# Optimization experiments

Hardware: AMD Instinct MI355X
Metric: run time of the kernel (lower is better)

The kernel has to match this reference:

```python
import jax, jax.numpy as jnp
import numpy as np

N, E, F, CUTOFF = 50000, 500000, 64, 5.0
EPS_CN, EPS_LN = 1e-8, 1e-5


def _xavier(k, shape):
    lim = float(np.sqrt(6.0 / (shape[0] + shape[1])))
    return jax.random.uniform(k, shape, jnp.float32, -lim, lim)


def setup_inputs() -> dict:
    key = jax.random.key(0)
    ks = jax.random.split(key, 20)
    vn = jax.random.normal(ks[5], (E, 3), jnp.float32)
    vn = vn / jnp.linalg.norm(vn, axis=-1, keepdims=True)  # unit direction vectors
    return {
        "node_s": jax.random.normal(ks[0], (N, 1, F), jnp.float32),
        "node_v": jax.random.normal(ks[1], (N, 3, F), jnp.float32),
        "edge_s": jax.random.normal(ks[2], (E, 1, F), jnp.float32),
        "edge_v": jax.random.normal(ks[3], (E, 3, F), jnp.float32),
        "dist": jax.random.uniform(ks[4], (E, 1), jnp.float32) * CUTOFF,
        "vctr_norm": vn,
        "src": jax.random.randint(ks[6], (E,), 0, N),
        "dst": jax.random.randint(ks[7], (E,), 0, N),
        "W_nn": _xavier(ks[8], (2 * F, F)), "b_nn": jnp.zeros((F,), jnp.float32),
        "W_ep": _xavier(ks[9], (F, F)), "b_ep": jnp.zeros((F,), jnp.float32),
        "W_g1": _xavier(ks[10], (F, F)), "b_g1": jnp.zeros((F,), jnp.float32),
        "W_g2": _xavier(ks[11], (F, F)), "b_g2": jnp.zeros((F,), jnp.float32),
        "W_ev": _xavier(ks[12], (F, 3 * F)), "b_ev": jnp.zeros((3 * F,), jnp.float32),
        "W_nvout": _xavier(ks[13], (F, 3 * F)),
        "W_nvc": _xavier(ks[14], (2 * F, F)), "b_nvc": jnp.zeros((F,), jnp.float32),
        "W_nvp": _xavier(ks[15], (F, 2 * F)),
        "W_nsp": _xavier(ks[16], (F, 2 * F)), "b_nsp": jnp.zeros((2 * F,), jnp.float32),
        "ln_gamma": jnp.ones((F,), jnp.float32), "ln_beta": jnp.zeros((F,), jnp.float32),
        "cn_scale": jnp.ones((F,), jnp.float32),
    }


def reference(node_s, node_v, edge_s, edge_v, dist, vctr_norm, src, dst,
              W_nn, b_nn, W_ep, b_ep, W_g1, b_g1, W_g2, b_g2, W_ev, b_ev,
              W_nvout, W_nvc, b_nvc, W_nvp, W_nsp, b_nsp, ln_gamma, ln_beta, cn_scale):
    n_nodes = node_s.shape[0]
    # cosine cutoff [E,1]
    c = 0.5 * (jnp.cos(jnp.pi * dist / CUTOFF) + 1.0) * (dist < CUTOFF).astype(dist.dtype)
    # ---- edge scalar update (gather src/dst, small MLPs) ----
    nn_in = jnp.concatenate([node_s[src], node_s[dst]], axis=-1)        # [E,1,2F]
    node_neighbors = nn_in @ W_nn + b_nn                                # [E,1,F]
    edge_message = node_neighbors * (edge_s @ W_ep + b_ep)              # [E,1,F]
    h = jax.nn.silu(edge_message @ W_g1 + b_g1)                         # GateMLP hidden
    es_upd = (h @ W_g2 + b_g2) * c[..., None]                           # [E,1,F]
    # ---- edge vector update ----
    vch = es_upd @ W_ev + b_ev                                          # [E,1,3F]
    nch, ech, rch = jnp.split(vch, 3, axis=-1)
    ev_upd = node_v[src] * nch + edge_v * ech + vctr_norm[..., None] * rch  # [E,3,F]
    ev_upd = ev_upd * c[..., None]
    # ---- scatter-mean to destination nodes ----
    deg = jax.ops.segment_sum(jnp.ones((src.shape[0],), node_s.dtype), dst, num_segments=n_nodes)
    denom = jnp.maximum(deg, 1.0)[:, None, None]
    n_ev = jax.ops.segment_sum(ev_upd, dst, num_segments=n_nodes) / denom  # [N,3,F]
    n_es = jax.ops.segment_sum(es_upd, dst, num_segments=n_nodes) / denom  # [N,1,F]
    # ---- node vector update ----
    nv_o1, nv_o2, nv_o3 = jnp.split(n_ev @ W_nvout, 3, axis=-1)          # each [N,3,F]
    v_in = jnp.concatenate([n_es, jnp.linalg.norm(nv_o3, axis=1, keepdims=True)], axis=-1)  # [N,1,2F]
    v_channel = v_in @ W_nvc + b_nvc                                     # [N,1,F]
    nv_upd = nv_o1 * v_channel + nv_o2                                   # [N,3,F]
    # ---- node scalar update ----
    nvp1, nvp2 = jnp.split(nv_upd @ W_nvp, 2, axis=-1)                   # [N,3,F] each
    ns1, ns2 = jnp.split(jax.nn.silu(n_es @ W_nsp + b_nsp), 2, axis=-1)  # [N,1,F] each
    nv_dot = jnp.sum(nvp1 * nvp2, axis=1, keepdims=True)                 # [N,1,F]
    ns_upd = nv_dot * ns1 + ns2                                          # [N,1,F]
    # ---- residuals + norms ----
    node_s_out = ns_upd + node_s
    node_v_out = nv_upd + node_v
    edge_s_out = es_upd + edge_s
    edge_v_out = ev_upd + edge_v
    # CoorsNorm: normalize over the 3D axis, learnable per-channel scale
    vnorm = jnp.linalg.norm(node_v_out, axis=1, keepdims=True)
    node_v_out = node_v_out / jnp.maximum(vnorm, EPS_CN) * cn_scale
    # LayerNorm over feature dim
    mu = jnp.mean(node_s_out, axis=-1, keepdims=True)
    var = jnp.var(node_s_out, axis=-1, keepdims=True)
    node_s_out = (node_s_out - mu) / jnp.sqrt(var + EPS_LN) * ln_gamma + ln_beta
    return node_s_out, node_v_out, edge_s_out, edge_v_out
```

## Files before the change

### kernel.cpp

```cpp
#include <hip/hip_runtime.h>
#include <hip/hip_bf16.h>
#include <math.h>

typedef __attribute__((ext_vector_type(8))) short bf16x8;
typedef __attribute__((ext_vector_type(4))) float f32x4;

#define MFMA16(a, b, c) __builtin_amdgcn_mfma_f32_16x16x32_bf16((a), (b), (c), 0, 0, 0)

__device__ __forceinline__ float silu_f(float x) { return x / (1.0f + expf(-x)); }

__device__ __forceinline__ unsigned short f2bf(float f) {
  union { __hip_bfloat16 h; unsigned short u; } c;
  c.h = __float2bfloat16(f);
  return c.u;
}
__device__ __forceinline__ unsigned pk2(float a, float b) {
  return (unsigned)f2bf(a) | ((unsigned)f2bf(b) << 16);
}
__device__ __forceinline__ float bfu(unsigned short u) {
  union { unsigned u32; float f; } c;
  c.u32 = (unsigned)u << 16;
  return c.f;
}

__device__ __forceinline__ bf16x8 ld_act(const unsigned short* buf, int strideB, int ks, int lane) {
  int row = lane & 15;
  int off = row * strideB + ks * 64 + ((lane >> 4) << 4);
  off ^= (row & 7) << 4;
  return *(const bf16x8*)((const char*)buf + off);
}

__device__ __forceinline__ bf16x8 ld_w(const unsigned short* Wt, int rowbase, int strideB, int ks, int lane) {
  return *(const bf16x8*)((const char*)Wt + (size_t)(rowbase + (lane & 15)) * strideB + ks * 64 + ((lane >> 4) << 4));
}

__global__ void wprep_all(const float* __restrict__ W_nn, const float* __restrict__ W_ep,
                          const float* __restrict__ W_g1, const float* __restrict__ W_g2,
                          const float* __restrict__ W_ev,
                          unsigned short* __restrict__ wnn_t, unsigned short* __restrict__ wep_t,
                          unsigned short* __restrict__ wg1_t, unsigned short* __restrict__ wg2_t,
                          unsigned short* __restrict__ wev_t) {
  int idx = blockIdx.x * 256 + threadIdx.x;
  if (idx < 8192) {
    int n = idx >> 7, k = idx & 127;
    wnn_t[idx] = f2bf(W_nn[k * 64 + n]);
  } else if (idx < 12288) {
    int t = idx - 8192; int n = t >> 6, k = t & 63;
    wep_t[t] = f2bf(W_ep[k * 64 + n]);
  } else if (idx < 16384) {
    int t = idx - 12288; int n = t >> 6, k = t & 63;
    wg1_t[t] = f2bf(W_g1[k * 64 + n]);
  } else if (idx < 20480) {
    int t = idx - 16384; int n = t >> 6, k = t & 63;
    wg2_t[t] = f2bf(W_g2[k * 64 + n]);
  } else if (idx < 32768) {
    int t = idx - 20480; int n = t >> 6, k = t & 63;
    wev_t[t] = f2bf(W_ev[k * 192 + n]);
  }
}

__global__ void hist_kernel(const int* __restrict__ dst, int* __restrict__ cnt, int E) {
  int i = blockIdx.x * blockDim.x + threadIdx.x;
  if (i < E) atomicAdd(&cnt[dst[i]], 1);
}

__global__ __launch_bounds__(1024) void scan_kernel(int* __restrict__ cnt,
                                                    int* __restrict__ rowstart, int N) {
  __shared__ int wsum[16];
  const int tid = threadIdx.x;
  const int wv = tid >> 6;
  int carry = 0;
  for (int base = 0; base < N; base += 1024) {
    int i = base + tid;
    int v = (i < N) ? cnt[i] : 0;
    int x = v;
    #pragma unroll
    for (int o = 1; o < 64; o <<= 1) {
      int y = __shfl_up(x, o);
      if ((tid & 63) >= o) x += y;
    }
    if ((tid & 63) == 63) wsum[wv] = x;
    __syncthreads();
    if (tid < 16) {
      int s = wsum[tid];
      #pragma unroll
      for (int o = 1; o < 16; o <<= 1) {
        int y = __shfl_up(s, o);
        if (tid >= o) s += y;
      }
      wsum[tid] = s;
    }
    __syncthreads();
    int woff = (wv > 0) ? wsum[wv - 1] : 0;
    if (i < N) {
      int excl = carry + woff + x - v;
      rowstart[i] = excl;
      cnt[i] = excl;
    }
    carry += wsum[15];
    __syncthreads();
  }
  if (tid == 0) rowstart[N] = carry;
}

__global__ void scatter_kernel(const int* __restrict__ dst, int* __restrict__ cursor,
                               int* __restrict__ elist, int E) {
  int i = blockIdx.x * blockDim.x + threadIdx.x;
  if (i < E) {
    int pos = atomicAdd(&cursor[dst[i]], 1);
    elist[pos] = i;
  }
}

__global__ __launch_bounds__(256, 8) void edge_kernel(
    const float* __restrict__ node_s, const float* __restrict__ node_v,
    const float* __restrict__ edge_s, const float* __restrict__ edge_v,
    const float* __restrict__ dist,   const float* __restrict__ vctr,
    const int* __restrict__ src,      const int* __restrict__ dst,
    const unsigned short* __restrict__ wnn_t, const float* __restrict__ b_nn,
    const unsigned short* __restrict__ wep_t, const float* __restrict__ b_ep,
    const unsigned short* __restrict__ wg1_t, const float* __restrict__ b_g1,
    const unsigned short* __restrict__ wg2_t, const float* __restrict__ b_g2,
    const unsigned short* __restrict__ wev_t, const float* __restrict__ b_ev,
    float* __restrict__ es_out, float* __restrict__ ev_out,
    unsigned short* __restrict__ raw_es, unsigned short* __restrict__ raw_ev,
    int use_raw, int E, int n_tiles)
{
  __shared__ __align__(16) unsigned short lds[4 * 2048];
  const int wid  = threadIdx.x >> 6;
  const int lane = threadIdx.x & 63;
  const int tile = blockIdx.x * 4 + wid;
  if (tile >= n_tiles) return;
  const int ebase = tile * 16;
  unsigned short* bufA = lds + wid * 2048;

  const int m  = lane & 15;
  const int nb = lane >> 4;

  {
    const int sm = lane >> 5;
    const int kk = lane & 31;
    #pragma unroll
    for (int p = 0; p < 8; ++p) {
      int le = p * 2 + sm;
      int e = ebase + le; if (e >= E) e = E - 1;
      int s = src[e], d = dst[e];
      float2 vs = *(const float2*)(node_s + (size_t)s * 64 + 2 * kk);
      float2 vd = *(const float2*)(node_s + (size_t)d * 64 + 2 * kk);
      unsigned swz = (le & 7) << 4;
      *(unsigned*)((char*)bufA + ((le * 256 + kk * 4) ^ swz))       = pk2(vs.x, vs.y);
      *(unsigned*)((char*)bufA + ((le * 256 + 128 + kk * 4) ^ swz)) = pk2(vd.x, vd.y);
    }
  }
  __builtin_amdgcn_wave_barrier();

  const int e = (ebase + m < E) ? ebase + m : E - 1;
  const float dd_ = dist[e];
  const float cc = (dd_ < 5.0f) ? 0.5f * (cosf(3.14159265358979f * dd_ * 0.2f) + 1.0f) : 0.0f;
  const int s_nd = src[e];

  const f32x4 z4 = {0.0f, 0.0f, 0.0f, 0.0f};
  const unsigned swzm = (m & 7) << 4;

  bf16x8 a0 = ld_act(bufA, 256, 0, lane), a1 = ld_act(bufA, 256, 1, lane);
  bf16x8 a2 = ld_act(bufA, 256, 2, lane), a3 = ld_act(bufA, 256, 3, lane);

  const float* esrow = edge_s + (size_t)e * 64;
  bf16x8 b0, b1;
  {
    const int k8 = (lane >> 4) << 3;
    f32x4 p0 = *(const f32x4*)(esrow + k8);
    f32x4 p1 = *(const f32x4*)(esrow + k8 + 4);
    f32x4 q0 = *(const f32x4*)(esrow + 32 + k8);
    f32x4 q1 = *(const f32x4*)(esrow + 32 + k8 + 4);
    union { bf16x8 v; uint4 u; } cb;
    cb.u.x = pk2(p0.x, p0.y); cb.u.y = pk2(p0.z, p0.w);
    cb.u.z = pk2(p1.x, p1.y); cb.u.w = pk2(p1.z, p1.w);
    b0 = cb.v;
    cb.u.x = pk2(q0.x, q0.y); cb.u.y = pk2(q0.z, q0.w);
    cb.u.z = pk2(q1.x, q1.y); cb.u.w = pk2(q1.z, q1.w);
    b1 = cb.v;
  }
  __builtin_amdgcn_wave_barrier();

  #pragma unroll
  for (int nt = 0; nt < 4; ++nt) {
    f32x4 aN = z4, aP = z4;
    aN = MFMA16(ld_w(wnn_t, nt * 16, 256, 0, lane), a0, aN);
    aN = MFMA16(ld_w(wnn_t, nt * 16, 256, 1, lane), a1, aN);
    aN = MFMA16(ld_w(wnn_t, nt * 16, 256, 2, lane), a2, aN);
    aN = MFMA16(ld_w(wnn_t, nt * 16, 256, 3, lane), a3, aN);
    aP = MFMA16(ld_w(wep_t, nt * 16, 128, 0, lane), b0, aP);
    aP = MFMA16(ld_w(wep_t, nt * 16, 128, 1, lane), b1, aP);
    f32x4 bn = *(const f32x4*)(b_nn + nt * 16 + nb * 4);
    f32x4 bp = *(const f32x4*)(b_ep + nt * 16 + nb * 4);
    float e0 = (aN.x + bn.x) * (aP.x + bp.x);
    float e1 = (aN.y + bn.y) * (aP.y + bp.y);
    float e2 = (aN.z + bn.z) * (aP.z + bp.z);
    float e3 = (aN.w + bn.w) * (aP.w + bp.w);
    uint2 w2; w2.x = pk2(e0, e1); w2.y = pk2(e2, e3);
    *(uint2*)((char*)bufA + ((m * 128 + nt * 32 + nb * 8) ^ swzm)) = w2;
  }
  __builtin_amdgcn_wave_barrier();

  bf16x8 c0 = ld_act(bufA, 128, 0, lane), c1 = ld_act(bufA, 128, 1, lane);
  __builtin_amdgcn_wave_barrier();
  #pragma unroll
  for (int nt = 0; nt < 4; ++nt) {
    f32x4 aH = z4;
    aH = MFMA16(ld_w(wg1_t, nt * 16, 128, 0, lane), c0, aH);
    aH = MFMA16(ld_w(wg1_t, nt * 16, 128, 1, lane), c1, aH);
    f32x4 bg = *(const f32x4*)(b_g1 + nt * 16 + nb * 4);
    uint2 w2;
    w2.x = pk2(silu_f(aH.x + bg.x), silu_f(aH.y + bg.y));
    w2.y = pk2(silu_f(aH.z + bg.z), silu_f(aH.w + bg.w));
    *(uint2*)((char*)bufA + ((m * 128 + nt * 32 + nb * 8) ^ swzm)) = w2;
  }
  __builtin_amdgcn_wave_barrier();

  bf16x8 d0 = ld_act(bufA, 128, 0, lane), d1 = ld_act(bufA, 128, 1, lane);
  __builtin_amdgcn_wave_barrier();
  float* eorow = es_out + (size_t)e * 64;
  #pragma unroll
  for (int nt = 0; nt < 4; ++nt) {
    f32x4 aS = z4;
    aS = MFMA16(ld_w(wg2_t, nt * 16, 128, 0, lane), d0, aS);
    aS = MFMA16(ld_w(wg2_t, nt * 16, 128, 1, lane), d1, aS);
    f32x4 bg = *(const f32x4*)(b_g2 + nt * 16 + nb * 4);
    float u0 = (aS.x + bg.x) * cc, u1 = (aS.y + bg.y) * cc;
    float u2 = (aS.z + bg.z) * cc, u3 = (aS.w + bg.w) * cc;
    const int n0 = nt * 16 + nb * 4;
    uint2 w2; w2.x = pk2(u0, u1); w2.y = pk2(u2, u3);
    *(uint2*)((char*)bufA + ((m * 128 + nt * 32 + nb * 8) ^ swzm)) = w2;
    if (use_raw) *(uint2*)(raw_es + (size_t)e * 64 + n0) = w2;
    if (ebase + m < E) {
      f32x4 r = *(const f32x4*)(esrow + n0);
      f32x4 o; o.x = u0 + r.x; o.y = u1 + r.y; o.z = u2 + r.z; o.w = u3 + r.w;
      __builtin_nontemporal_store(o, (f32x4*)(eorow + n0));
    }
  }
  __builtin_amdgcn_wave_barrier();

  bf16x8 g0 = ld_act(bufA, 128, 0, lane), g1f = ld_act(bufA, 128, 1, lane);
  const float* nvb = node_v + (size_t)s_nd * 192;
  const float* evb = edge_v + (size_t)e * 192;
  float* eob = ev_out + (size_t)e * 192;
  float vnn0 = vctr[e * 3], vnn1 = vctr[e * 3 + 1], vnn2 = vctr[e * 3 + 2];
  const bool live = (ebase + m < E);
  #pragma unroll
  for (int nt = 0; nt < 4; ++nt) {
    f32x4 aN = z4, aE = z4, aR = z4;
    aN = MFMA16(ld_w(wev_t,        nt * 16, 128, 0, lane), g0,  aN);
    aN = MFMA16(ld_w(wev_t,        nt * 16, 128, 1, lane), g1f, aN);
    aE = MFMA16(ld_w(wev_t,  64 + nt * 16, 128, 0, lane), g0,  aE);
    aE = MFMA16(ld_w(wev_t,  64 + nt * 16, 128, 1, lane), g1f, aE);
    aR = MFMA16(ld_w(wev_t, 128 + nt * 16, 128, 0, lane), g0,  aR);
    aR = MFMA16(ld_w(wev_t, 128 + nt * 16, 128, 1, lane), g1f, aR);
    const int n0 = nt * 16 + nb * 4;
    f32x4 bv0 = *(const f32x4*)(b_ev + n0);
    f32x4 bv1 = *(const f32x4*)(b_ev + 64 + n0);
    f32x4 bv2 = *(const f32x4*)(b_ev + 128 + n0);
    aN.x += bv0.x; aN.y += bv0.y; aN.z += bv0.z; aN.w += bv0.w;
    aE.x += bv1.x; aE.y += bv1.y; aE.z += bv1.z; aE.w += bv1.w;
    aR.x += bv2.x; aR.y += bv2.y; aR.z += bv2.z; aR.w += bv2.w;
    #pragma unroll
    for (int dd = 0; dd < 3; ++dd) {
      const float vn = (dd == 0) ? vnn0 : (dd == 1) ? vnn1 : vnn2;
      f32x4 nv = *(const f32x4*)(nvb + dd * 64 + n0);
      f32x4 ev = __builtin_nontemporal_load((const f32x4*)(evb + dd * 64 + n0));
      float eu0 = (nv.x * aN.x + ev.x * aE.x + vn * aR.x) * cc;
      float eu1 = (nv.y * aN.y + ev.y * aE.y + vn * aR.y) * cc;
      float eu2 = (nv.z * aN.z + ev.z * aE.z + vn * aR.z) * cc;
      float eu3 = (nv.w * aN.w + ev.w * aE.w + vn * aR.w) * cc;
      if (use_raw) {
        uint2 r; r.x = pk2(eu0, eu1); r.y = pk2(eu2, eu3);
        *(uint2*)(raw_ev + (size_t)e * 192 + dd * 64 + n0) = r;
      }
      if (live) {
        f32x4 o; o.x = eu0 + ev.x; o.y = eu1 + ev.y; o.z = eu2 + ev.z; o.w = eu3 + ev.w;
        __builtin_nontemporal_store(o, (f32x4*)(eob + dd * 64 + n0));
      }
    }
  }
}

__device__ __forceinline__ void ld4(const float* p, float o[4]) {
  f32x4 v = *(const f32x4*)p;
  o[0] = v.x; o[1] = v.y; o[2] = v.z; o[3] = v.w;
}

__global__ __launch_bounds__(256) void node_kernel(
    const float* __restrict__ node_s, const float* __restrict__ node_v,
    const float* __restrict__ edge_s, const float* __restrict__ edge_v,
    const float* __restrict__ es_r,   const float* __restrict__ ev_r,
    const unsigned short* __restrict__ raw_es, const unsigned short* __restrict__ raw_ev,
    const int* __restrict__ rowstart, const int* __restrict__ elist, int use_raw,
    const float* __restrict__ W_nvout,
    const float* __restrict__ W_nvc, const float* __restrict__ b_nvc,
    const float* __restrict__ W_nvp,
    const float* __restrict__ W_nsp, const float* __restrict__ b_nsp,
    const float* __restrict__ ln_g, const float* __restrict__ ln_b,
    const float* __restrict__ cn_s,
    float* __restrict__ ns_out, float* __restrict__ nv_out, int N)
{
  __shared__ __align__(16) float scm[4 * 8 * 68];
  const int wid = threadIdx.x >> 6, lane = threadIdx.x & 63;
  const int n = blockIdx.x * 4 + wid;
  if (n >= N) return;
  float* S = &scm[wid * 8 * 68];

  const int rs = rowstart[n], re = rowstart[n + 1];
  float nes = 0.0f, nev0 = 0.0f, nev1 = 0.0f, nev2 = 0.0f;
  if (use_raw) {
    int idx = rs;
    for (; idx + 1 < re; idx += 2) {
      int ea = elist[idx], eb = elist[idx + 1];
      const unsigned short* pa = raw_es + (size_t)ea * 64 + lane;
      const unsigned short* pb = raw_es + (size_t)eb * 64 + lane;
      const unsigned short* va = raw_ev + (size_t)ea * 192 + lane;
      const unsigned short* vb = raw_ev + (size_t)eb * 192 + lane;
      unsigned short x0 = pa[0], x1 = pb[0];
      unsigned short a0 = va[0], a1 = va[64], a2 = va[128];
      unsigned short b0 = vb[0], b1 = vb[64], b2 = vb[128];
      nes  += bfu(x0) + bfu(x1);
      nev0 += bfu(a0) + bfu(b0);
      nev1 += bfu(a1) + bfu(b1);
      nev2 += bfu(a2) + bfu(b2);
    }
    if (idx < re) {
      int ea = elist[idx];
      nes  += bfu(raw_es[(size_t)ea * 64 + lane]);
      const unsigned short* va = raw_ev + (size_t)ea * 192 + lane;
      nev0 += bfu(va[0]); nev1 += bfu(va[64]); nev2 += bfu(va[128]);
    }
  } else {
    for (int idx = rs; idx < re; ++idx) {
      int e = elist[idx];
      size_t b64 = (size_t)e * 64, b192 = (size_t)e * 192;
      nes  += es_r[b64 + lane]        - edge_s[b64 + lane];
      nev0 += ev_r[b192 + lane]       - edge_v[b192 + lane];
      nev1 += ev_r[b192 + 64 + lane]  - edge_v[b192 + 64 + lane];
      nev2 += ev_r[b192 + 128 + lane] - edge_v[b192 + 128 + lane];
    }
  }
  const float inv = 1.0f / fmaxf((float)(re - rs), 1.0f);
  nes *= inv; nev0 *= inv; nev1 *= inv; nev2 *= inv;

  S[0 * 68 + lane] = nev0; S[1 * 68 + lane] = nev1;
  S[2 * 68 + lane] = nev2; S[3 * 68 + lane] = nes;
  __builtin_amdgcn_wave_barrier();

  float o1[3] = {}, o2[3] = {}, o3[3] = {};
  for (int k = 0; k < 64; k += 4) {
    float a0[4], a1[4], a2[4];
    ld4(S + 0 * 68 + k, a0); ld4(S + 1 * 68 + k, a1); ld4(S + 2 * 68 + k, a2);
    #pragma unroll
    for (int kk = 0; kk < 4; ++kk) {
      float w0 = W_nvout[(k + kk) * 192 + lane];
      float w1 = W_nvout[(k + kk) * 192 + 64 + lane];
      float w2 = W_nvout[(k + kk) * 192 + 128 + lane];
      o1[0] = fmaf(a0[kk], w0, o1[0]); o1[1] = fmaf(a1[kk], w0, o1[1]); o1[2] = fmaf(a2[kk], w0, o1[2]);
      o2[0] = fmaf(a0[kk], w1, o2[0]); o2[1] = fmaf(a1[kk], w1, o2[1]); o2[2] = fmaf(a2[kk], w1, o2[2]);
      o3[0] = fmaf(a0[kk], w2, o3[0]); o3[1] = fmaf(a1[kk], w2, o3[1]); o3[2] = fmaf(a2[kk], w2, o3[2]);
    }
  }
  float nrm = sqrtf(o3[0] * o3[0] + o3[1] * o3[1] + o3[2] * o3[2]);
  S[4 * 68 + lane] = nrm;
  __builtin_amdgcn_wave_barrier();

  float vch = 0.0f;
  for (int k = 0; k < 64; k += 4) {
    float a[4], b[4];
    ld4(S + 3 * 68 + k, a); ld4(S + 4 * 68 + k, b);
    #pragma unroll
    for (int kk = 0; kk < 4; ++kk) {
      vch = fmaf(a[kk], W_nvc[(k + kk) * 64 + lane], vch);
      vch = fmaf(b[kk], W_nvc[(64 + k + kk) * 64 + lane], vch);
    }
  }
  vch += b_nvc[lane];

  float nvu[3];
  #pragma unroll
  for (int dd = 0; dd < 3; ++dd) {
    nvu[dd] = o1[dd] * vch + o2[dd];
    S[(5 + dd) * 68 + lane] = nvu[dd];
  }
  __builtin_amdgcn_wave_barrier();

  float p1[3] = {}, p2[3] = {};
  for (int k = 0; k < 64; k += 4) {
    float a0[4], a1[4], a2[4];
    ld4(S + 5 * 68 + k, a0); ld4(S + 6 * 68 + k, a1); ld4(S + 7 * 68 + k, a2);
    #pragma unroll
    for (int kk = 0; kk < 4; ++kk) {
      float w1 = W_nvp[(k + kk) * 128 + lane];
      float w2 = W_nvp[(k + kk) * 128 + 64 + lane];
      p1[0] = fmaf(a0[kk], w1, p1[0]); p1[1] = fmaf(a1[kk], w1, p1[1]); p1[2] = fmaf(a2[kk], w1, p1[2]);
      p2[0] = fmaf(a0[kk], w2, p2[0]); p2[1] = fmaf(a1[kk], w2, p2[1]); p2[2] = fmaf(a2[kk], w2, p2[2]);
    }
  }

  float s1a = 0.0f, s2a = 0.0f;
  for (int k = 0; k < 64; k += 4) {
    float a[4];
    ld4(S + 3 * 68 + k, a);
    #pragma unroll
    for (int kk = 0; kk < 4; ++kk) {
      s1a = fmaf(a[kk], W_nsp[(k + kk) * 128 + lane], s1a);
      s2a = fmaf(a[kk], W_nsp[(k + kk) * 128 + 64 + lane], s2a);
    }
  }
  float s1 = silu_f(s1a + b_nsp[lane]);
  float s2 = silu_f(s2a + b_nsp[64 + lane]);

  float nvdot = p1[0] * p2[0] + p1[1] * p2[1] + p1[2] * p2[2];
  float nsu = nvdot * s1 + s2;

  float xs = nsu + node_s[n * 64 + lane];
  float sum = xs, sumsq = xs * xs;
  #pragma unroll
  for (int o = 32; o; o >>= 1) {
    sum += __shfl_xor(sum, o);
    sumsq += __shfl_xor(sumsq, o);
  }
  float mu = sum * (1.0f / 64.0f);
  float var = sumsq * (1.0f / 64.0f) - mu * mu;
  ns_out[n * 64 + lane] = (xs - mu) * rsqrtf(var + 1e-5f) * ln_g[lane] + ln_b[lane];

  float vv[3];
  #pragma unroll
  for (int dd = 0; dd < 3; ++dd) vv[dd] = nvu[dd] + node_v[n * 192 + dd * 64 + lane];
  float vn2 = sqrtf(vv[0] * vv[0] + vv[1] * vv[1] + vv[2] * vv[2]);
  float scale = cn_s[lane] / fmaxf(vn2, 1e-8f);
  #pragma unroll
  for (int dd = 0; dd < 3; ++dd)
    nv_out[n * 192 + dd * 64 + lane] = vv[dd] * scale;
}

extern "C" void kernel_launch(void* const* d_in, const int* in_sizes, int n_in,
                              void* d_out, int out_size, void* d_ws, size_t ws_size,
                              hipStream_t stream) {
  const float* node_s = (const float*)d_in[0];
  const float* node_v = (const float*)d_in[1];
  const float* edge_s = (const float*)d_in[2];
  const float* edge_v = (const float*)d_in[3];
  const float* dist   = (const float*)d_in[4];
  const float* vctr   = (const float*)d_in[5];
  const int*   src    = (const int*)d_in[6];
  const int*   dst    = (const int*)d_in[7];
  const float* W_nn = (const float*)d_in[8];  const float* b_nn = (const float*)d_in[9];
  const float* W_ep = (const float*)d_in[10]; const float* b_ep = (const float*)d_in[11];
  const float* W_g1 = (const float*)d_in[12]; const float* b_g1 = (const float*)d_in[13];
  const float* W_g2 = (const float*)d_in[14]; const float* b_g2 = (const float*)d_in[15];
  const float* W_ev = (const float*)d_in[16]; const float* b_ev = (const float*)d_in[17];
  const float* W_nvout = (const float*)d_in[18];
  const float* W_nvc = (const float*)d_in[19]; const float* b_nvc = (const float*)d_in[20];
  const float* W_nvp = (const float*)d_in[21];
  const float* W_nsp = (const float*)d_in[22]; const float* b_nsp = (const float*)d_in[23];
  const float* ln_g = (const float*)d_in[24]; const float* ln_b = (const float*)d_in[25];
  const float* cn_s = (const float*)d_in[26];

  const int N = in_sizes[0] / 64;
  const int E = in_sizes[2] / 64;

  float* out    = (float*)d_out;
  float* ns_out = out;
  float* nv_out = out + (size_t)N * 64;
  float* es_out = out + (size_t)N * 256;
  float* ev_out = out + (size_t)N * 256 + (size_t)E * 64;

  int* cnt      = (int*)d_ws;
  int* rowstart = cnt + N;
  int* elist    = rowstart + N + 1;
  unsigned short* wnn_t = (unsigned short*)(elist + E);
  unsigned short* wep_t = wnn_t + 64 * 128;
  unsigned short* wg1_t = wep_t + 64 * 64;
  unsigned short* wg2_t = wg1_t + 64 * 64;
  unsigned short* wev_t = wg2_t + 64 * 64;
  size_t wend = (size_t)((char*)(wev_t + 192 * 64) - (char*)d_ws);
  size_t rawofs = (wend + 255) & ~(size_t)255;
  unsigned short* raw_es = (unsigned short*)((char*)d_ws + rawofs);
  unsigned short* raw_ev = raw_es + (size_t)E * 64;
  size_t need = rawofs + (size_t)E * 256 * sizeof(unsigned short);
  int use_raw = (ws_size >= need) ? 1 : 0;

  hipMemsetAsync(cnt, 0, (size_t)N * sizeof(int), stream);
  hist_kernel<<<(E + 255) / 256, 256, 0, stream>>>(dst, cnt, E);
  scan_kernel<<<1, 1024, 0, stream>>>(cnt, rowstart, N);
  scatter_kernel<<<(E + 255) / 256, 256, 0, stream>>>(dst, cnt, elist, E);

  wprep_all<<<128, 256, 0, stream>>>(W_nn, W_ep, W_g1, W_g2, W_ev,
                                     wnn_t, wep_t, wg1_t, wg2_t, wev_t);

  int n_tiles = (E + 15) / 16;
  edge_kernel<<<(n_tiles + 3) / 4, 256, 0, stream>>>(
      node_s, node_v, edge_s, edge_v, dist, vctr, src, dst,
      wnn_t, b_nn, wep_t, b_ep, wg1_t, b_g1, wg2_t, b_g2, wev_t, b_ev,
      es_out, ev_out, raw_es, raw_ev, use_raw, E, n_tiles);

  node_kernel<<<(N + 3) / 4, 256, 0, stream>>>(
      node_s, node_v, edge_s, edge_v, es_out, ev_out, raw_es, raw_ev,
      rowstart, elist, use_raw,
      W_nvout, W_nvc, b_nvc, W_nvp, W_nsp, b_nsp,
      ln_g, ln_b, cn_s, ns_out, nv_out, N);
}
```

Before: 1.137 ms.

## Write raw edge updates in dst-sorted order so node gather reads contiguously

The scatter kernel now records each edge's position in the dst-sorted list. The edge kernel uses it to write its bf16 scalar and vector updates straight to sorted slots, with the vector update split into three planes and staged through LDS as full 16-byte rows. The node kernel can then stream its edges contiguously instead of chasing elist indices. In exchange, the edge kernel's output writes become scattered, it needs more registers (all 12 vector accumulators are held at once, and launch bounds drop to 4 blocks), and it adds an extra epos array and extra LDS traffic.

```diff
diff --git a/kernel.cpp b/kernel.cpp
--- a/kernel.cpp
+++ b/kernel.cpp
@@ -104,19 +104,21 @@
 }
 
 __global__ void scatter_kernel(const int* __restrict__ dst, int* __restrict__ cursor,
-                               int* __restrict__ elist, int E) {
+                               int* __restrict__ elist, int* __restrict__ epos, int E) {
   int i = blockIdx.x * blockDim.x + threadIdx.x;
   if (i < E) {
     int pos = atomicAdd(&cursor[dst[i]], 1);
     elist[pos] = i;
-  }
-}
-
-__global__ __launch_bounds__(256, 8) void edge_kernel(
+    epos[i] = pos;
+  }
+}
+
+__global__ __launch_bounds__(256, 4) void edge_kernel(
     const float* __restrict__ node_s, const float* __restrict__ node_v,
     const float* __restrict__ edge_s, const float* __restrict__ edge_v,
     const float* __restrict__ dist,   const float* __restrict__ vctr,
     const int* __restrict__ src,      const int* __restrict__ dst,
+    const int* __restrict__ epos,
     const unsigned short* __restrict__ wnn_t, const float* __restrict__ b_nn,
     const unsigned short* __restrict__ wep_t, const float* __restrict__ b_ep,
     const unsigned short* __restrict__ wg1_t, const float* __restrict__ b_g1,
@@ -133,6 +135,7 @@
   if (tile >= n_tiles) return;
   const int ebase = tile * 16;
   unsigned short* bufA = lds + wid * 2048;
+  const size_t Estride = (size_t)E * 64;
 
   const int m  = lane & 15;
   const int nb = lane >> 4;
@@ -161,6 +164,14 @@
 
   const f32x4 z4 = {0.0f, 0.0f, 0.0f, 0.0f};
   const unsigned swzm = (m & 7) << 4;
+
+  const int tme  = lane >> 3;
+  const int tseg = lane & 7;
+  int tpos0 = -1, tpos1 = -1;
+  if (use_raw) {
+    if (ebase + tme < E)     tpos0 = epos[ebase + tme];
+    if (ebase + 8 + tme < E) tpos1 = epos[ebase + 8 + tme];
+  }
 
   bf16x8 a0 = ld_act(bufA, 256, 0, lane), a1 = ld_act(bufA, 256, 1, lane);
   bf16x8 a2 = ld_act(bufA, 256, 2, lane), a3 = ld_act(bufA, 256, 3, lane);
@@ -232,7 +243,6 @@
     const int n0 = nt * 16 + nb * 4;
     uint2 w2; w2.x = pk2(u0, u1); w2.y = pk2(u2, u3);
     *(uint2*)((char*)bufA + ((m * 128 + nt * 32 + nb * 8) ^ swzm)) = w2;
-    if (use_raw) *(uint2*)(raw_es + (size_t)e * 64 + n0) = w2;
     if (ebase + m < E) {
       f32x4 r = *(const f32x4*)(esrow + n0);
       f32x4 o; o.x = u0 + r.x; o.y = u1 + r.y; o.z = u2 + r.z; o.w = u3 + r.w;
@@ -242,43 +252,64 @@
   __builtin_amdgcn_wave_barrier();
 
   bf16x8 g0 = ld_act(bufA, 128, 0, lane), g1f = ld_act(bufA, 128, 1, lane);
+  if (use_raw) {
+    if (tpos0 >= 0) {
+      bf16x8 row = *(const bf16x8*)((const char*)bufA + ((tme * 128 + tseg * 16) ^ ((tme & 7) << 4)));
+      *(bf16x8*)(raw_es + (size_t)tpos0 * 64 + tseg * 8) = row;
+    }
+    if (tpos1 >= 0) {
+      bf16x8 row = *(const bf16x8*)((const char*)bufA + (((8 + tme) * 128 + tseg * 16) ^ (((8 + tme) & 7) << 4)));
+      *(bf16x8*)(raw_es + (size_t)tpos1 * 64 + tseg * 8) = row;
+    }
+  }
+
+  f32x4 accV[12];
+  #pragma unroll
+  for (int ch = 0; ch < 3; ++ch)
+    #pragma unroll
+    for (int nt = 0; nt < 4; ++nt) {
+      f32x4 a = z4;
+      a = MFMA16(ld_w(wev_t, ch * 64 + nt * 16, 128, 0, lane), g0,  a);
+      a = MFMA16(ld_w(wev_t, ch * 64 + nt * 16, 128, 1, lane), g1f, a);
+      f32x4 bv = *(const f32x4*)(b_ev + ch * 64 + nt * 16 + nb * 4);
+      a.x += bv.x; a.y += bv.y; a.z += bv.z; a.w += bv.w;
+      accV[ch * 4 + nt] = a;
+    }
+
   const float* nvb = node_v + (size_t)s_nd * 192;
   const float* evb = edge_v + (size_t)e * 192;
   float* eob = ev_out + (size_t)e * 192;
-  float vnn0 = vctr[e * 3], vnn1 = vctr[e * 3 + 1], vnn2 = vctr[e * 3 + 2];
+  const float vnn[3] = {vctr[e * 3], vctr[e * 3 + 1], vctr[e * 3 + 2]};
   const bool live = (ebase + m < E);
   #pragma unroll
-  for (int nt = 0; nt < 4; ++nt) {
-    f32x4 aN = z4, aE = z4, aR = z4;
-    aN = MFMA16(ld_w(wev_t,        nt * 16, 128, 0, lane), g0,  aN);
-    aN = MFMA16(ld_w(wev_t,        nt * 16, 128, 1, lane), g1f, aN);
-    aE = MFMA16(ld_w(wev_t,  64 + nt * 16, 128, 0, lane), g0,  aE);
-    aE = MFMA16(ld_w(wev_t,  64 + nt * 16, 128, 1, lane), g1f, aE);
-    aR = MFMA16(ld_w(wev_t, 128 + nt * 16, 128, 0, lane), g0,  aR);
-    aR = MFMA16(ld_w(wev_t, 128 + nt * 16, 128, 1, lane), g1f, aR);
-    const int n0 = nt * 16 + nb * 4;
-    f32x4 bv0 = *(const f32x4*)(b_ev + n0);
-    f32x4 bv1 = *(const f32x4*)(b_ev + 64 + n0);
-    f32x4 bv2 = *(const f32x4*)(b_ev + 128 + n0);
-    aN.x += bv0.x; aN.y += bv0.y; aN.z += bv0.z; aN.w += bv0.w;
-    aE.x += bv1.x; aE.y += bv1.y; aE.z += bv1.z; aE.w += bv1.w;
-    aR.x += bv2.x; aR.y += bv2.y; aR.z += bv2.z; aR.w += bv2.w;
-    #pragma unroll
-    for (int dd = 0; dd < 3; ++dd) {
-      const float vn = (dd == 0) ? vnn0 : (dd == 1) ? vnn1 : vnn2;
+  for (int dd = 0; dd < 3; ++dd) {
+    __builtin_amdgcn_wave_barrier();
+    #pragma unroll
+    for (int nt = 0; nt < 4; ++nt) {
+      const int n0 = nt * 16 + nb * 4;
       f32x4 nv = *(const f32x4*)(nvb + dd * 64 + n0);
       f32x4 ev = __builtin_nontemporal_load((const f32x4*)(evb + dd * 64 + n0));
-      float eu0 = (nv.x * aN.x + ev.x * aE.x + vn * aR.x) * cc;
-      float eu1 = (nv.y * aN.y + ev.y * aE.y + vn * aR.y) * cc;
-      float eu2 = (nv.z * aN.z + ev.z * aE.z + vn * aR.z) * cc;
-      float eu3 = (nv.w * aN.w + ev.w * aE.w + vn * aR.w) * cc;
-      if (use_raw) {
-        uint2 r; r.x = pk2(eu0, eu1); r.y = pk2(eu2, eu3);
-        *(uint2*)(raw_ev + (size_t)e * 192 + dd * 64 + n0) = r;
-      }
+      float eu0 = (nv.x * accV[nt].x + ev.x * accV[4 + nt].x + vnn[dd] * accV[8 + nt].x) * cc;
+      float eu1 = (nv.y * accV[nt].y + ev.y * accV[4 + nt].y + vnn[dd] * accV[8 + nt].y) * cc;
+      float eu2 = (nv.z * accV[nt].z + ev.z * accV[4 + nt].z + vnn[dd] * accV[8 + nt].z) * cc;
+      float eu3 = (nv.w * accV[nt].w + ev.w * accV[4 + nt].w + vnn[dd] * accV[8 + nt].w) * cc;
       if (live) {
         f32x4 o; o.x = eu0 + ev.x; o.y = eu1 + ev.y; o.z = eu2 + ev.z; o.w = eu3 + ev.w;
         __builtin_nontemporal_store(o, (f32x4*)(eob + dd * 64 + n0));
+      }
+      uint2 w2; w2.x = pk2(eu0, eu1); w2.y = pk2(eu2, eu3);
+      *(uint2*)((char*)bufA + ((m * 128 + nt * 32 + nb * 8) ^ swzm)) = w2;
+    }
+    __builtin_amdgcn_wave_barrier();
+    if (use_raw) {
+      unsigned short* plane = raw_ev + (size_t)dd * Estride;
+      if (tpos0 >= 0) {
+        bf16x8 row = *(const bf16x8*)((const char*)bufA + ((tme * 128 + tseg * 16) ^ ((tme & 7) << 4)));
+        *(bf16x8*)(plane + (size_t)tpos0 * 64 + tseg * 8) = row;
+      }
+      if (tpos1 >= 0) {
+        bf16x8 row = *(const bf16x8*)((const char*)bufA + (((8 + tme) * 128 + tseg * 16) ^ (((8 + tme) & 7) << 4)));
+        *(bf16x8*)(plane + (size_t)tpos1 * 64 + tseg * 8) = row;
       }
     }
   }
@@ -301,7 +332,7 @@
     const float* __restrict__ W_nsp, const float* __restrict__ b_nsp,
     const float* __restrict__ ln_g, const float* __restrict__ ln_b,
     const float* __restrict__ cn_s,
-    float* __restrict__ ns_out, float* __restrict__ nv_out, int N)
+    float* __restrict__ ns_out, float* __restrict__ nv_out, int N, int E)
 {
   __shared__ __align__(16) float scm[4 * 8 * 68];
   const int wid = threadIdx.x >> 6, lane = threadIdx.x & 63;
@@ -312,26 +343,26 @@
   const int rs = rowstart[n], re = rowstart[n + 1];
   float nes = 0.0f, nev0 = 0.0f, nev1 = 0.0f, nev2 = 0.0f;
   if (use_raw) {
-    int idx = rs;
-    for (; idx + 1 < re; idx += 2) {
-      int ea = elist[idx], eb = elist[idx + 1];
-      const unsigned short* pa = raw_es + (size_t)ea * 64 + lane;
-      const unsigned short* pb = raw_es + (size_t)eb * 64 + lane;
-      const unsigned short* va = raw_ev + (size_t)ea * 192 + lane;
-      const unsigned short* vb = raw_ev + (size_t)eb * 192 + lane;
-      unsigned short x0 = pa[0], x1 = pb[0];
-      unsigned short a0 = va[0], a1 = va[64], a2 = va[128];
-      unsigned short b0 = vb[0], b1 = vb[64], b2 = vb[128];
-      nes  += bfu(x0) + bfu(x1);
-      nev0 += bfu(a0) + bfu(b0);
-      nev1 += bfu(a1) + bfu(b1);
-      nev2 += bfu(a2) + bfu(b2);
-    }
-    if (idx < re) {
-      int ea = elist[idx];
-      nes  += bfu(raw_es[(size_t)ea * 64 + lane]);
-      const unsigned short* va = raw_ev + (size_t)ea * 192 + lane;
-      nev0 += bfu(va[0]); nev1 += bfu(va[64]); nev2 += bfu(va[128]);
+    const size_t Estride = (size_t)E * 64;
+    const unsigned short* pe = raw_es + (size_t)rs * 64 + lane;
+    const unsigned short* v0 = raw_ev + (size_t)rs * 64 + lane;
+    const unsigned short* v1 = v0 + Estride;
+    const unsigned short* v2 = v1 + Estride;
+    const int cntE = re - rs;
+    int i = 0;
+    for (; i + 1 < cntE; i += 2) {
+      unsigned short e0 = pe[i * 64],  e1 = pe[i * 64 + 64];
+      unsigned short a0 = v0[i * 64],  a1 = v0[i * 64 + 64];
+      unsigned short b0 = v1[i * 64],  b1 = v1[i * 64 + 64];
+      unsigned short c0 = v2[i * 64],  c1 = v2[i * 64 + 64];
+      nes  += bfu(e0) + bfu(e1);
+      nev0 += bfu(a0) + bfu(a1);
+      nev1 += bfu(b0) + bfu(b1);
+      nev2 += bfu(c0) + bfu(c1);
+    }
+    if (i < cntE) {
+      nes  += bfu(pe[i * 64]);
+      nev0 += bfu(v0[i * 64]); nev1 += bfu(v1[i * 64]); nev2 += bfu(v2[i * 64]);
     }
   } else {
     for (int idx = rs; idx < re; ++idx) {
@@ -472,7 +503,8 @@
 
   int* cnt      = (int*)d_ws;
   int* rowstart = cnt + N;
-  int* elist    = rowstart + N + 1;
+  int* epos     = rowstart + N + 1;
+  int* elist    = epos + E;
   unsigned short* wnn_t = (unsigned short*)(elist + E);
   unsigned short* wep_t = wnn_t + 64 * 128;
   unsigned short* wg1_t = wep_t + 64 * 64;
@@ -488,14 +520,14 @@
   hipMemsetAsync(cnt, 0, (size_t)N * sizeof(int), stream);
   hist_kernel<<<(E + 255) / 256, 256, 0, stream>>>(dst, cnt, E);
   scan_kernel<<<1, 1024, 0, stream>>>(cnt, rowstart, N);
-  scatter_kernel<<<(E + 255) / 256, 256, 0, stream>>>(dst, cnt, elist, E);
+  scatter_kernel<<<(E + 255) / 256, 256, 0, stream>>>(dst, cnt, elist, epos, E);
 
   wprep_all<<<128, 256, 0, stream>>>(W_nn, W_ep, W_g1, W_g2, W_ev,
                                      wnn_t, wep_t, wg1_t, wg2_t, wev_t);
 
   int n_tiles = (E + 15) / 16;
   edge_kernel<<<(n_tiles + 3) / 4, 256, 0, stream>>>(
-      node_s, node_v, edge_s, edge_v, dist, vctr, src, dst,
+      node_s, node_v, edge_s, edge_v, dist, vctr, src, dst, epos,
       wnn_t, b_nn, wep_t, b_ep, wg1_t, b_g1, wg2_t, b_g2, wev_t, b_ev,
       es_out, ev_out, raw_es, raw_ev, use_raw, E, n_tiles);
 
@@ -503,5 +535,5 @@
       node_s, node_v, edge_s, edge_v, es_out, ev_out, raw_es, raw_ev,
       rowstart, elist, use_raw,
       W_nvout, W_nvc, b_nvc, W_nvp, W_nsp, b_nsp,
-      ln_g, ln_b, cn_s, ns_out, nv_out, N);
-}
+      ln_g, ln_b, cn_s, ns_out, nv_out, N, E);
+}
```

Measured after the change: 993.7 us. -12.6%, faster.
